# Optimization experiments

Measured on AMD Instinct MI355X. Metric: run time of the kernel, lower is better.

The kernel has to match this reference:

```python
import jax, jax.numpy as jnp
import numpy as np

NPOINT = 1024
RADIUS = 0.2
NSAMPLE = 32
MLP = (64, 64, 128)
EPS = 1e-5  # torch BatchNorm2d default


def farthest_point_sample(xyz, npoint):
    """xyz: [B,N,3] -> centroid indices [B,npoint] (deterministic start at index 0)."""
    B, N, _ = xyz.shape

    def step(carry, _):
        distance, farthest = carry  # [B,N], [B]
        centroid = jnp.take_along_axis(xyz, farthest[:, None, None], axis=1)  # [B,1,3]
        dist = jnp.sum((xyz - centroid) ** 2, axis=-1)  # [B,N]
        distance = jnp.minimum(distance, dist)
        new_farthest = jnp.argmax(distance, axis=-1)
        return (distance, new_farthest), farthest

    init = (jnp.full((B, N), 1e10, xyz.dtype), jnp.zeros((B,), jnp.int32))
    _, centroids = jax.lax.scan(step, init, None, length=npoint)  # [npoint,B]
    return centroids.T  # [B,npoint]


def ball_query(xyz, new_xyz, radius, nsample):
    """xyz:[B,N,3], new_xyz:[B,M,3] -> group_idx [B,M,nsample]."""
    N = xyz.shape[1]
    # sqrdists[b,m,n] = ||new_xyz[b,m] - xyz[b,n]||^2
    sqrdists = jnp.sum((new_xyz[:, :, None, :] - xyz[:, None, :, :]) ** 2, axis=-1)  # [B,M,N]
    idx = jnp.where(sqrdists > radius * radius, N, jnp.arange(N, dtype=jnp.int32))
    idx = jnp.sort(idx, axis=-1)[:, :, :nsample]
    return jnp.where(idx == N, 0, idx)  # out-of-ball slots fall back to point 0 (as in source)


def index_points(points, idx):
    """points:[B,N,C], idx:[B,M,K] -> [B,M,K,C]."""
    B, M, K = idx.shape
    flat = idx.reshape(B, M * K)
    out = jnp.take_along_axis(points, flat[:, :, None], axis=1)
    return out.reshape(B, M, K, points.shape[-1])


def _forward(xyz, points, layers):
    B = xyz.shape[0]
    fps_idx = farthest_point_sample(xyz, NPOINT)
    new_xyz = jnp.take_along_axis(xyz, fps_idx[:, :, None], axis=1)  # [B,M,3]
    group_idx = ball_query(xyz, new_xyz, RADIUS, NSAMPLE)  # [B,M,K]
    grouped_xyz = index_points(xyz, group_idx) - new_xyz[:, :, None, :]  # [B,M,K,3]
    x = jnp.concatenate([grouped_xyz, index_points(points, group_idx)], axis=-1)  # [B,M,K,3+C]
    # shared MLP: 1x1 conv + BatchNorm (training-mode batch stats) + ReLU
    for (w, b, g, be) in layers:
        x = jnp.einsum('bmkc,oc->bmko', x, w) + b
        mean = jnp.mean(x, axis=(0, 1, 2))
        var = jnp.var(x, axis=(0, 1, 2))  # biased, matches torch BN normalization
        x = jax.nn.relu(g * (x - mean) * jax.lax.rsqrt(var + EPS) + be)
    new_points = jnp.max(x, axis=2)  # [B,M,Cout]
    return new_xyz, new_points


def setup_inputs() -> dict:
    key = jax.random.key(0)
    ks = jax.random.split(key, 2 + len(MLP))
    B, N, C = 16, 4096, 64
    inp = {
        'xyz': jax.random.uniform(ks[0], (B, N, 3), jnp.float32),
        'points': jax.random.normal(ks[1], (B, N, C), jnp.float32),
    }
    last = 3 + C
    for i, out_ch in enumerate(MLP):
        inp[f'w{i}'] = jax.random.normal(ks[2 + i], (out_ch, last), jnp.float32) / np.sqrt(last).astype(np.float32)
        inp[f'b{i}'] = jnp.zeros((out_ch,), jnp.float32)
        inp[f'g{i}'] = jnp.ones((out_ch,), jnp.float32)
        inp[f'be{i}'] = jnp.zeros((out_ch,), jnp.float32)
        last = out_ch
    return inp


def reference(xyz, points, w0, b0, g0, be0, w1, b1, g1, be1, w2, b2, g2, be2):
    layers = [(w0, b0, g0, be0), (w1, b1, g1, be1), (w2, b2, g2, be2)]
    return _forward(xyz, points, layers)
```

## Files before the change

kernel.cpp:

```cpp
#include <hip/hip_runtime.h>

typedef unsigned int uint;
typedef unsigned short ushort;
typedef unsigned long long u64;

#define N_PTS 4096
#define B_SZ 16
#define M_PTS 1024
#define K_SMP 32
#define NROWS (B_SZ*M_PTS*K_SMP)
#define INV_CNT (1.0f/524288.0f)

__device__ __forceinline__ float sqdist3(float ax,float ay,float az,float bx,float by,float bz){
  float dx=__fsub_rn(ax,bx), dy=__fsub_rn(ay,by), dz=__fsub_rn(az,bz);
  return __fadd_rn(__fadd_rn(__fmul_rn(dx,dx),__fmul_rn(dy,dy)),__fmul_rn(dz,dz));
}
__device__ __forceinline__ ushort f2bf(float x){
  uint u = __float_as_uint(x);
  u = (u + 0x7fffu + ((u>>16)&1u)) >> 16;
  return (ushort)u;
}
__device__ __forceinline__ float bf2f(uint u){ return __uint_as_float(u<<16); }

__device__ __forceinline__ void kmerge(uint& kl, uint& kh, uint okl, uint okh){
  u64 a = ((u64)kh << 32) | kl;
  u64 b = ((u64)okh << 32) | okl;
  bool t = b > a;
  kl = t ? okl : kl;
  kh = t ? okh : kh;
}
template<int CTRL>
__device__ __forceinline__ uint dppu(uint v){
  return (uint)__builtin_amdgcn_update_dpp((int)v, (int)v, CTRL, 0xf, 0xf, false);
}
template<int CTRL>
__device__ __forceinline__ void dppkmerge(uint& kl, uint& kh){
  uint okl = dppu<CTRL>(kl);
  uint okh = dppu<CTRL>(kh);
  kmerge(kl, kh, okl, okh);
}

__global__ __launch_bounds__(512, 2) void fps_kernel(const float* __restrict__ xyz,
                                                     float* __restrict__ out_newxyz){
  const int b = blockIdx.x;
  const int t = threadIdx.x;
  __shared__ float4 sxyz[N_PTS];
  __shared__ uint   xch[2][8][2];
  const float* src = xyz + (size_t)b*N_PTS*3;
  float px[8], py[8], pz[8], dist[8];
  uint nl[8];
#pragma unroll
  for (int i=0;i<8;i++){
    const int p = t + 512*i;
    float x = src[3*p+0], y = src[3*p+1], z = src[3*p+2];
    px[i]=x; py[i]=y; pz[i]=z;
    dist[i]=1e10f; nl[i] = ~(uint)p;
    sxyz[p] = make_float4(x, y, z, 0.f);
  }
  __syncthreads();
  float cx, cy, cz;
  { float4 c0 = sxyz[0]; cx=c0.x; cy=c0.y; cz=c0.z; }
  const int w = t >> 6, lane = t & 63;
  float* outx = out_newxyz + (size_t)b*M_PTS*3;
  for (int s = 0; s < M_PTS; ++s){
    if (t == 0){ outx[s*3+0]=cx; outx[s*3+1]=cy; outx[s*3+2]=cz; }
    uint khv[8];
#pragma unroll
    for (int i=0;i<8;i++){
      float d  = sqdist3(px[i],py[i],pz[i],cx,cy,cz);
      float nd = fminf(dist[i], d);
      dist[i] = nd;
      khv[i] = __float_as_uint(nd);
    }
    uint l0=nl[0], h0=khv[0]; kmerge(l0,h0,nl[1],khv[1]);
    uint l1=nl[2], h1=khv[2]; kmerge(l1,h1,nl[3],khv[3]);
    uint l2=nl[4], h2=khv[4]; kmerge(l2,h2,nl[5],khv[5]);
    uint l3=nl[6], h3=khv[6]; kmerge(l3,h3,nl[7],khv[7]);
    kmerge(l0,h0,l1,h1); kmerge(l2,h2,l3,h3); kmerge(l0,h0,l2,h2);
    uint al=l0, ah=h0;
    dppkmerge<0x111>(al, ah);
    dppkmerge<0x112>(al, ah);
    dppkmerge<0x114>(al, ah);
    dppkmerge<0x118>(al, ah);
    dppkmerge<0x142>(al, ah);
    dppkmerge<0x143>(al, ah);
    const int par = s & 1;
    if (lane == 63){ xch[par][w][0] = al; xch[par][w][1] = ah; }
    __syncthreads();
    uint ckl = xch[par][lane & 7][0];
    uint ckh = xch[par][lane & 7][1];
    dppkmerge<0x111>(ckl, ckh);
    dppkmerge<0x112>(ckl, ckh);
    dppkmerge<0x114>(ckl, ckh);
    uint wkl = (uint)__builtin_amdgcn_readlane((int)ckl, 7);
    uint idx = ~wkl;
    float4 cc = sxyz[idx];
    cx = cc.x; cy = cc.y; cz = cc.z;
  }
}

__global__ __launch_bounds__(256) void ballq_kernel(const float* __restrict__ xyz,
                                                    const float* __restrict__ newxyz,
                                                    int* __restrict__ gidx){
  const int blk = blockIdx.x;
  const int b = blk >> 6;
  const int mbase = (blk & 63) * 16;
  __shared__ float sx[N_PTS], sy[N_PTS], sz[N_PTS];
  const float* src = xyz + (size_t)b*N_PTS*3;
  for (int i = threadIdx.x; i < N_PTS*3; i += 256){
    float v = src[i]; int p = i/3, j = i%3;
    (j==0?sx:(j==1?sy:sz))[p] = v;
  }
  __syncthreads();
  const int w = threadIdx.x >> 6, lane = threadIdx.x & 63;
  const float R2 = (float)(0.2*0.2);
  for (int mm = w; mm < 16; mm += 4){
    const int m = mbase + mm;
    const float* c = newxyz + ((size_t)b*M_PTS + m)*3;
    float cx = c[0], cy = c[1], cz = c[2];
    int* gout = gidx + ((size_t)b*M_PTS + m)*K_SMP;
    int cnt = 0;
    for (int base = 0; base < N_PTS && cnt < K_SMP; base += 64){
      int p = base + lane;
      float d = sqdist3(sx[p],sy[p],sz[p],cx,cy,cz);
      bool in = (d <= R2);
      unsigned long long mask = __ballot(in);
      int prefix = __popcll(mask & ((1ull << lane) - 1ull));
      int slot = cnt + prefix;
      if (in && slot < K_SMP) gout[slot] = p;
      cnt += __popcll(mask);
    }
    if (cnt < K_SMP){
      int slot = cnt + lane;
      if (slot < K_SMP) gout[slot] = 0;
    }
  }
}

__global__ __launch_bounds__(256, 2) void conv0_kernel(const float* __restrict__ xyz,
                                                       const float* __restrict__ points,
                                                       const float* __restrict__ newxyz,
                                                       const int* __restrict__ gidx,
                                                       const float* __restrict__ W0,
                                                       const float* __restrict__ b0,
                                                       ushort* __restrict__ x1){
  __shared__ float A [67][132];
  __shared__ float Bw[67][68];
  __shared__ float sb[64];
  const int tid = threadIdx.x;
  if (tid < 64) sb[tid] = b0[tid];
  for (int idx = tid; idx < 64*67; idx += 256){
    int o = idx / 67, k = idx - o*67;
    Bw[k][o] = W0[idx];
  }
  const size_t rbase = (size_t)blockIdx.x * 128;
  {
    const int r  = tid & 127;
    const int hf = tid >> 7;
    const int R = (int)rbase + r;
    const int b_ = R >> 15, m_ = (R >> 5) & 1023;
    const int g_ = gidx[R];
    const float4* p4 = (const float4*)(points + (((size_t)(b_<<12) + g_) << 6) + hf*32);
#pragma unroll
    for (int j=0;j<8;j++){
      float4 v = p4[j];
      int c = 3 + hf*32 + j*4;
      A[c+0][r]=v.x; A[c+1][r]=v.y; A[c+2][r]=v.z; A[c+3][r]=v.w;
    }
    if (hf == 0){
      const float* pc = newxyz + ((size_t)(b_<<10) + m_)*3;
      const float* pp = xyz    + ((size_t)(b_<<12) + g_)*3;
      A[0][r] = pp[0]-pc[0];
      A[1][r] = pp[1]-pc[1];
      A[2][r] = pp[2]-pc[2];
    }
  }
  __syncthreads();
  const int tr = tid >> 4, tc = tid & 15;
  float acc[8][4];
#pragma unroll
  for (int i=0;i<8;i++)
#pragma unroll
    for (int j=0;j<4;j++) acc[i][j] = sb[tc*4+j];
#pragma unroll 4
  for (int k=0;k<67;k++){
    float4 a0 = *(const float4*)&A [k][tr*8];
    float4 a1 = *(const float4*)&A [k][tr*8+4];
    float4 w  = *(const float4*)&Bw[k][tc*4];
    float av[8] = {a0.x,a0.y,a0.z,a0.w,a1.x,a1.y,a1.z,a1.w};
#pragma unroll
    for (int i=0;i<8;i++){
      acc[i][0]=fmaf(av[i],w.x,acc[i][0]);
      acc[i][1]=fmaf(av[i],w.y,acc[i][1]);
      acc[i][2]=fmaf(av[i],w.z,acc[i][2]);
      acc[i][3]=fmaf(av[i],w.w,acc[i][3]);
    }
  }
#pragma unroll
  for (int i=0;i<8;i++){
    uint2 v;
    v.x = (uint)f2bf(acc[i][0]) | ((uint)f2bf(acc[i][1])<<16);
    v.y = (uint)f2bf(acc[i][2]) | ((uint)f2bf(acc[i][3])<<16);
    *(uint2*)(x1 + ((rbase + tr*8 + i) << 6) + tc*4) = v;
  }
}

__global__ __launch_bounds__(256, 2) void convg64_kernel(const ushort* __restrict__ xin,
                                                         const float* __restrict__ Sv,
                                                         const float* __restrict__ SSv,
                                                         const float* __restrict__ gg,
                                                         const float* __restrict__ be,
                                                         const float* __restrict__ W,
                                                         const float* __restrict__ bias,
                                                         ushort* __restrict__ xout){
  __shared__ float A [64][132];
  __shared__ float Bw[64][68];
  __shared__ float sc[64], sh[64], sb[64];
  const int tid = threadIdx.x;
  if (tid < 64){
    int c = tid;
    float mean = Sv[c]*INV_CNT;
    float var  = fmaf(-mean, mean, SSv[c]*INV_CNT);
    float is   = rsqrtf(var + 1e-5f);
    float scv  = gg[c]*is;
    sc[c] = scv; sh[c] = fmaf(-mean, scv, be[c]);
    sb[c] = bias[c];
  }
  {
    const int o  = tid & 63;
    const int kq = tid >> 6;
    const float* wrow = W + (size_t)o*64 + kq*16;
#pragma unroll
    for (int q=0;q<4;q++){
      float4 wv = *(const float4*)(wrow + q*4);
      int k = kq*16 + q*4;
      Bw[k+0][o]=wv.x; Bw[k+1][o]=wv.y; Bw[k+2][o]=wv.z; Bw[k+3][o]=wv.w;
    }
  }
  __syncthreads();
  const size_t rbase = (size_t)blockIdx.x * 128;
  {
    const int r  = tid & 127;
    const int kh = tid >> 7;
    const uint4* src = (const uint4*)(xin + ((rbase + r) << 6) + kh*32);
#pragma unroll
    for (int g=0; g<4; g++){
      uint4 v = src[g];
      uint d[4] = {v.x,v.y,v.z,v.w};
#pragma unroll
      for (int q=0;q<4;q++){
        int k = kh*32 + g*8 + 2*q;
        float a0 = bf2f(d[q] & 0xffffu), a1 = bf2f(d[q] >> 16);
        A[k+0][r] = fmaxf(fmaf(a0, sc[k+0], sh[k+0]), 0.f);
        A[k+1][r] = fmaxf(fmaf(a1, sc[k+1], sh[k+1]), 0.f);
      }
    }
  }
  __syncthreads();
  const int tr = tid >> 4, tc = tid & 15;
  float acc[8][4];
#pragma unroll
  for (int i=0;i<8;i++)
#pragma unroll
    for (int j=0;j<4;j++) acc[i][j] = sb[tc*4+j];
#pragma unroll 4
  for (int k=0;k<64;k++){
    float4 a0 = *(const float4*)&A [k][tr*8];
    float4 a1 = *(const float4*)&A [k][tr*8+4];
    float4 w  = *(const float4*)&Bw[k][tc*4];
    float av[8] = {a0.x,a0.y,a0.z,a0.w,a1.x,a1.y,a1.z,a1.w};
#pragma unroll
    for (int i=0;i<8;i++){
      acc[i][0]=fmaf(av[i],w.x,acc[i][0]);
      acc[i][1]=fmaf(av[i],w.y,acc[i][1]);
      acc[i][2]=fmaf(av[i],w.z,acc[i][2]);
      acc[i][3]=fmaf(av[i],w.w,acc[i][3]);
    }
  }
#pragma unroll
  for (int i=0;i<8;i++){
    uint2 v;
    v.x = (uint)f2bf(acc[i][0]) | ((uint)f2bf(acc[i][1])<<16);
    v.y = (uint)f2bf(acc[i][2]) | ((uint)f2bf(acc[i][3])<<16);
    *(uint2*)(xout + ((rbase + tr*8 + i) << 6) + tc*4) = v;
  }
}

__global__ __launch_bounds__(256, 2) void convg128_kernel(const ushort* __restrict__ xin,
                                                          const float* __restrict__ Sv,
                                                          const float* __restrict__ SSv,
                                                          const float* __restrict__ gg,
                                                          const float* __restrict__ be,
                                                          const float* __restrict__ W,
                                                          const float* __restrict__ bias,
                                                          ushort* __restrict__ xout){
  __shared__ float A [64][132];
  __shared__ float Bw[64][132];
  __shared__ float sc[64], sh[64], sb[128];
  const int tid = threadIdx.x;
  if (tid < 64){
    int c = tid;
    float mean = Sv[c]*INV_CNT;
    float var  = fmaf(-mean, mean, SSv[c]*INV_CNT);
    float is   = rsqrtf(var + 1e-5f);
    float scv  = gg[c]*is;
    sc[c] = scv; sh[c] = fmaf(-mean, scv, be[c]);
  }
  if (tid < 128) sb[tid] = bias[tid];
  {
    const int o  = tid & 127;
    const int kh = tid >> 7;
    const float* wrow = W + (size_t)o*64 + kh*32;
#pragma unroll
    for (int q=0;q<8;q++){
      float4 wv = *(const float4*)(wrow + q*4);
      int k = kh*32 + q*4;
      Bw[k+0][o]=wv.x; Bw[k+1][o]=wv.y; Bw[k+2][o]=wv.z; Bw[k+3][o]=wv.w;
    }
  }
  __syncthreads();
  const size_t rbase = (size_t)blockIdx.x * 128;
  {
    const int r  = tid & 127;
    const int kh = tid >> 7;
    const uint4* src = (const uint4*)(xin + ((rbase + r) << 6) + kh*32);
#pragma unroll
    for (int g=0; g<4; g++){
      uint4 v = src[g];
      uint d[4] = {v.x,v.y,v.z,v.w};
#pragma unroll
      for (int q=0;q<4;q++){
        int k = kh*32 + g*8 + 2*q;
        float a0 = bf2f(d[q] & 0xffffu), a1 = bf2f(d[q] >> 16);
        A[k+0][r] = fmaxf(fmaf(a0, sc[k+0], sh[k+0]), 0.f);
        A[k+1][r] = fmaxf(fmaf(a1, sc[k+1], sh[k+1]), 0.f);
      }
    }
  }
  __syncthreads();
  const int tr = tid >> 4, tc = tid & 15;
  float acc[8][8];
#pragma unroll
  for (int i=0;i<8;i++)
#pragma unroll
    for (int j=0;j<8;j++) acc[i][j] = sb[tc*8+j];
#pragma unroll 2
  for (int k=0;k<64;k++){
    float4 a0 = *(const float4*)&A [k][tr*8];
    float4 a1 = *(const float4*)&A [k][tr*8+4];
    float4 w0 = *(const float4*)&Bw[k][tc*8];
    float4 w1 = *(const float4*)&Bw[k][tc*8+4];
    float av[8] = {a0.x,a0.y,a0.z,a0.w,a1.x,a1.y,a1.z,a1.w};
    float wv[8] = {w0.x,w0.y,w0.z,w0.w,w1.x,w1.y,w1.z,w1.w};
#pragma unroll
    for (int i=0;i<8;i++)
#pragma unroll
      for (int j=0;j<8;j++)
        acc[i][j] = fmaf(av[i], wv[j], acc[i][j]);
  }
#pragma unroll
  for (int i=0;i<8;i++){
    uint4 v;
    v.x = (uint)f2bf(acc[i][0]) | ((uint)f2bf(acc[i][1])<<16);
    v.y = (uint)f2bf(acc[i][2]) | ((uint)f2bf(acc[i][3])<<16);
    v.z = (uint)f2bf(acc[i][4]) | ((uint)f2bf(acc[i][5])<<16);
    v.w = (uint)f2bf(acc[i][6]) | ((uint)f2bf(acc[i][7])<<16);
    *(uint4*)(xout + ((rbase + tr*8 + i) << 7) + tc*8) = v;
  }
}

template<int C>
__global__ __launch_bounds__(256) void stats_kernel(const ushort* __restrict__ x,
                                                    float* __restrict__ S,
                                                    float* __restrict__ SS){
  constexpr int GRP = C/8;
  constexpr int RL  = 256/GRP;
  const int cg = threadIdx.x % GRP;
  const int rl = threadIdx.x / GRP;
  const int rows_per_block = NROWS / 1024;
  const int r0 = blockIdx.x * rows_per_block;
  float s[8], ss[8];
#pragma unroll
  for (int j=0;j<8;j++){ s[j]=0.f; ss[j]=0.f; }
  for (int r = r0 + rl; r < r0 + rows_per_block; r += RL){
    uint4 v = *(const uint4*)(x + (size_t)r*C + cg*8);
    uint d[4] = {v.x, v.y, v.z, v.w};
#pragma unroll
    for (int q=0;q<4;q++){
      float a0 = bf2f(d[q] & 0xffffu), a1 = bf2f(d[q] >> 16);
      s[2*q]   += a0; ss[2*q]   = fmaf(a0, a0, ss[2*q]);
      s[2*q+1] += a1; ss[2*q+1] = fmaf(a1, a1, ss[2*q+1]);
    }
  }
  __shared__ float ls[256][8], lss[256][8];
#pragma unroll
  for (int j=0;j<8;j++){ ls[threadIdx.x][j]=s[j]; lss[threadIdx.x][j]=ss[j]; }
  __syncthreads();
  if (threadIdx.x < C){
    const int grp = threadIdx.x >> 3, j = threadIdx.x & 7;
    float a = 0.f, q2 = 0.f;
#pragma unroll
    for (int q = 0; q < RL; q++){ a += ls[q*GRP + grp][j]; q2 += lss[q*GRP + grp][j]; }
    atomicAdd(&S[threadIdx.x], a); atomicAdd(&SS[threadIdx.x], q2);
  }
}

__global__ __launch_bounds__(256) void maxpool_kernel(const ushort* __restrict__ x3,
                                                      const float* __restrict__ S2,
                                                      const float* __restrict__ SS2,
                                                      const float* __restrict__ g2,
                                                      const float* __restrict__ be2,
                                                      float* __restrict__ outp){
  const int lane = threadIdx.x & 63, wv = threadIdx.x >> 6;
  const int bm = blockIdx.x*4 + wv;
  const int c0 = lane*2, c1 = c0+1;
  float mean0 = S2[c0]*INV_CNT;
  float var0  = fmaf(-mean0, mean0, SS2[c0]*INV_CNT);
  float s0 = g2[c0]*rsqrtf(var0+1e-5f);
  float h0 = fmaf(-mean0, s0, be2[c0]);
  float mean1 = S2[c1]*INV_CNT;
  float var1  = fmaf(-mean1, mean1, SS2[c1]*INV_CNT);
  float s1 = g2[c1]*rsqrtf(var1+1e-5f);
  float h1 = fmaf(-mean1, s1, be2[c1]);
  const uint* rb = (const uint*)(x3 + (size_t)bm*K_SMP*128);
  float mx0 = 0.f, mx1 = 0.f;
#pragma unroll
  for (int k=0;k<K_SMP;k++){
    uint v = rb[k*64 + lane];
    float a0 = bf2f(v & 0xffffu), a1 = bf2f(v >> 16);
    mx0 = fmaxf(mx0, fmaxf(fmaf(a0, s0, h0), 0.f));
    mx1 = fmaxf(mx1, fmaxf(fmaf(a1, s1, h1), 0.f));
  }
  float2* o2 = (float2*)(outp + (size_t)bm*128);
  o2[lane] = make_float2(mx0, mx1);
}

extern "C" void kernel_launch(void* const* d_in, const int* in_sizes, int n_in,
                              void* d_out, int out_size, void* d_ws, size_t ws_size,
                              hipStream_t stream){
  const float* xyz    = (const float*)d_in[0];
  const float* points = (const float*)d_in[1];
  const float* w0  = (const float*)d_in[2];
  const float* b0  = (const float*)d_in[3];
  const float* g0  = (const float*)d_in[4];
  const float* be0 = (const float*)d_in[5];
  const float* w1  = (const float*)d_in[6];
  const float* b1  = (const float*)d_in[7];
  const float* g1  = (const float*)d_in[8];
  const float* be1 = (const float*)d_in[9];
  const float* w2  = (const float*)d_in[10];
  const float* b2  = (const float*)d_in[11];
  const float* g2  = (const float*)d_in[12];
  const float* be2 = (const float*)d_in[13];

  float* out      = (float*)d_out;
  float* newxyz   = out;
  float* outp     = out + (size_t)B_SZ*M_PTS*3;

  char* ws = (char*)d_ws;
  int*   gidx  = (int*)ws;
  float* stats = (float*)(ws + (2u<<20));
  float* S0 = stats,      *SS0 = stats+64;
  float* S1 = stats+128,  *SS1 = stats+192;
  float* S2 = stats+256,  *SS2 = stats+384;
  ushort* x1 = (ushort*)(ws + (4u<<20));
  ushort* x3 = (ushort*)(ws + (4u<<20));
  ushort* x2 = (ushort*)(ws + (4u<<20) + 134217728u);

  hipMemsetAsync(stats, 0, 512*sizeof(float), stream);
  fps_kernel  <<<B_SZ, 512, 0, stream>>>(xyz, newxyz);
  ballq_kernel<<<1024, 256, 0, stream>>>(xyz, newxyz, gidx);
  conv0_kernel<<<NROWS/128, 256, 0, stream>>>(xyz, points, newxyz, gidx, w0, b0, x1);
  stats_kernel<64><<<1024, 256, 0, stream>>>(x1, S0, SS0);
  convg64_kernel<<<NROWS/128, 256, 0, stream>>>(x1, S0, SS0, g0, be0, w1, b1, x2);
  stats_kernel<64><<<1024, 256, 0, stream>>>(x2, S1, SS1);
  convg128_kernel<<<NROWS/128, 256, 0, stream>>>(x2, S1, SS1, g1, be1, w2, b2, x3);
  stats_kernel<128><<<1024, 256, 0, stream>>>(x3, S2, SS2);
  maxpool_kernel<<<NROWS/128, 256, 0, stream>>>(x3, S2, SS2, g2, be2, outp);
}
```

Measured before the change: 1.102 ms.

## Fuse BN stats into conv kernels and simplify FPS argmax reduction

The BatchNorm sum and sum-of-squares for the first two layers are now accumulated in the conv0 and convg64 epilogues from the bf16-rounded outputs and reduced with shuffles, shared memory and atomics. This removes two separate stats kernels that each re-read a large intermediate tensor. FPS also changes: each thread now owns 8 contiguous points loaded with float4 reads, and the per-step argmax uses a float max reduction plus a ballot and readlane instead of 64-bit packed key merges. Ties are resolved by a first-index search, but float atomics make the stats summation order nondeterministic.

```diff
diff --git a/kernel.cpp b/kernel.cpp
--- a/kernel.cpp
+++ b/kernel.cpp
@@ -22,22 +22,22 @@
 }
 __device__ __forceinline__ float bf2f(uint u){ return __uint_as_float(u<<16); }
 
-__device__ __forceinline__ void kmerge(uint& kl, uint& kh, uint okl, uint okh){
-  u64 a = ((u64)kh << 32) | kl;
-  u64 b = ((u64)okh << 32) | okl;
-  bool t = b > a;
-  kl = t ? okl : kl;
-  kh = t ? okh : kh;
-}
 template<int CTRL>
 __device__ __forceinline__ uint dppu(uint v){
   return (uint)__builtin_amdgcn_update_dpp((int)v, (int)v, CTRL, 0xf, 0xf, false);
 }
 template<int CTRL>
-__device__ __forceinline__ void dppkmerge(uint& kl, uint& kh){
-  uint okl = dppu<CTRL>(kl);
-  uint okh = dppu<CTRL>(kh);
-  kmerge(kl, kh, okl, okh);
+__device__ __forceinline__ float dppmaxf(float v){
+  float o = __uint_as_float(dppu<CTRL>(__float_as_uint(v)));
+  return fmaxf(v, o);
+}
+template<int CTRL>
+__device__ __forceinline__ void dppscan(float& v, uint& i){
+  float ov = __uint_as_float(dppu<CTRL>(__float_as_uint(v)));
+  uint  oi = dppu<CTRL>(i);
+  bool tk = (ov >= v);
+  v = tk ? ov : v;
+  i = tk ? oi : i;
 }
 
 __global__ __launch_bounds__(512, 2) void fps_kernel(const float* __restrict__ xyz,
@@ -45,17 +45,23 @@
   const int b = blockIdx.x;
   const int t = threadIdx.x;
   __shared__ float4 sxyz[N_PTS];
-  __shared__ uint   xch[2][8][2];
+  __shared__ __align__(8) uint2 xch[2][8];
   const float* src = xyz + (size_t)b*N_PTS*3;
+  for (int i = t; i < N_PTS; i += 512)
+    sxyz[i] = make_float4(src[3*i], src[3*i+1], src[3*i+2], 0.f);
+  const int p0 = t*8;
   float px[8], py[8], pz[8], dist[8];
-  uint nl[8];
-#pragma unroll
-  for (int i=0;i<8;i++){
-    const int p = t + 512*i;
-    float x = src[3*p+0], y = src[3*p+1], z = src[3*p+2];
-    px[i]=x; py[i]=y; pz[i]=z;
-    dist[i]=1e10f; nl[i] = ~(uint)p;
-    sxyz[p] = make_float4(x, y, z, 0.f);
+  {
+    const float4* s4 = (const float4*)(src + 3*p0);
+    float4 v[6];
+#pragma unroll
+    for (int q=0;q<6;q++) v[q] = s4[q];
+    const float* f = (const float*)v;
+#pragma unroll
+    for (int i=0;i<8;i++){
+      px[i]=f[3*i]; py[i]=f[3*i+1]; pz[i]=f[3*i+2];
+      dist[i]=1e10f;
+    }
   }
   __syncthreads();
   float cx, cy, cz;
@@ -64,37 +70,43 @@
   float* outx = out_newxyz + (size_t)b*M_PTS*3;
   for (int s = 0; s < M_PTS; ++s){
     if (t == 0){ outx[s*3+0]=cx; outx[s*3+1]=cy; outx[s*3+2]=cz; }
-    uint khv[8];
 #pragma unroll
     for (int i=0;i<8;i++){
-      float d  = sqdist3(px[i],py[i],pz[i],cx,cy,cz);
-      float nd = fminf(dist[i], d);
-      dist[i] = nd;
-      khv[i] = __float_as_uint(nd);
-    }
-    uint l0=nl[0], h0=khv[0]; kmerge(l0,h0,nl[1],khv[1]);
-    uint l1=nl[2], h1=khv[2]; kmerge(l1,h1,nl[3],khv[3]);
-    uint l2=nl[4], h2=khv[4]; kmerge(l2,h2,nl[5],khv[5]);
-    uint l3=nl[6], h3=khv[6]; kmerge(l3,h3,nl[7],khv[7]);
-    kmerge(l0,h0,l1,h1); kmerge(l2,h2,l3,h3); kmerge(l0,h0,l2,h2);
-    uint al=l0, ah=h0;
-    dppkmerge<0x111>(al, ah);
-    dppkmerge<0x112>(al, ah);
-    dppkmerge<0x114>(al, ah);
-    dppkmerge<0x118>(al, ah);
-    dppkmerge<0x142>(al, ah);
-    dppkmerge<0x143>(al, ah);
+      float d = sqdist3(px[i],py[i],pz[i],cx,cy,cz);
+      dist[i] = fminf(dist[i], d);
+    }
+    float m8 = fmaxf(fmaxf(fmaxf(dist[0],dist[1]), fmaxf(dist[2],dist[3])),
+                     fmaxf(fmaxf(dist[4],dist[5]), fmaxf(dist[6],dist[7])));
+    uint li = 7;
+    if (dist[6] == m8) li = 6;
+    if (dist[5] == m8) li = 5;
+    if (dist[4] == m8) li = 4;
+    if (dist[3] == m8) li = 3;
+    if (dist[2] == m8) li = 2;
+    if (dist[1] == m8) li = 1;
+    if (dist[0] == m8) li = 0;
+    const uint gi = (uint)p0 + li;
+    float wm = m8;
+    wm = dppmaxf<0x111>(wm);
+    wm = dppmaxf<0x112>(wm);
+    wm = dppmaxf<0x114>(wm);
+    wm = dppmaxf<0x118>(wm);
+    wm = dppmaxf<0x142>(wm);
+    wm = dppmaxf<0x143>(wm);
+    const float M = __uint_as_float((uint)__builtin_amdgcn_readlane((int)__float_as_uint(wm), 63));
+    unsigned long long blt = __ballot(m8 == M);
+    const int ll = __builtin_ctzll(blt);
+    const uint widx = (uint)__builtin_amdgcn_readlane((int)gi, ll);
     const int par = s & 1;
-    if (lane == 63){ xch[par][w][0] = al; xch[par][w][1] = ah; }
+    if (lane == 63) xch[par][w] = make_uint2(__float_as_uint(M), widx);
     __syncthreads();
-    uint ckl = xch[par][lane & 7][0];
-    uint ckh = xch[par][lane & 7][1];
-    dppkmerge<0x111>(ckl, ckh);
-    dppkmerge<0x112>(ckl, ckh);
-    dppkmerge<0x114>(ckl, ckh);
-    uint wkl = (uint)__builtin_amdgcn_readlane((int)ckl, 7);
-    uint idx = ~wkl;
-    float4 cc = sxyz[idx];
+    uint2 cw = xch[par][lane & 7];
+    float cv = __uint_as_float(cw.x); uint ci = cw.y;
+    dppscan<0x111>(cv, ci);
+    dppscan<0x112>(cv, ci);
+    dppscan<0x114>(cv, ci);
+    uint fi = (uint)__builtin_amdgcn_readlane((int)ci, 7);
+    float4 cc = sxyz[fi];
     cx = cc.x; cy = cc.y; cz = cc.z;
   }
 }
@@ -137,16 +149,40 @@
   }
 }
 
+__device__ __forceinline__ void conv_stats64(float s[4], float q[4], float (*sred)[16][8],
+                                             int tid, float* S, float* SS){
+  const int lane = tid & 63, w = tid >> 6, tc = tid & 15;
+#pragma unroll
+  for (int j=0;j<4;j++){
+    s[j] += __shfl_xor(s[j], 16); s[j] += __shfl_xor(s[j], 32);
+    q[j] += __shfl_xor(q[j], 16); q[j] += __shfl_xor(q[j], 32);
+  }
+  if (lane < 16){
+#pragma unroll
+    for (int j=0;j<4;j++){ sred[w][tc][j] = s[j]; sred[w][tc][4+j] = q[j]; }
+  }
+  __syncthreads();
+  if (tid < 64){
+    const int tcg = tid >> 2, j = tid & 3;
+    float a = sred[0][tcg][j]   + sred[1][tcg][j]   + sred[2][tcg][j]   + sred[3][tcg][j];
+    float b = sred[0][tcg][4+j] + sred[1][tcg][4+j] + sred[2][tcg][4+j] + sred[3][tcg][4+j];
+    atomicAdd(&S[tid], a); atomicAdd(&SS[tid], b);
+  }
+}
+
 __global__ __launch_bounds__(256, 2) void conv0_kernel(const float* __restrict__ xyz,
                                                        const float* __restrict__ points,
                                                        const float* __restrict__ newxyz,
                                                        const int* __restrict__ gidx,
                                                        const float* __restrict__ W0,
                                                        const float* __restrict__ b0,
-                                                       ushort* __restrict__ x1){
+                                                       ushort* __restrict__ x1,
+                                                       float* __restrict__ S0,
+                                                       float* __restrict__ SS0){
   __shared__ float A [67][132];
   __shared__ float Bw[67][68];
   __shared__ float sb[64];
+  __shared__ float sred[4][16][8];
   const int tid = threadIdx.x;
   if (tid < 64) sb[tid] = b0[tid];
   for (int idx = tid; idx < 64*67; idx += 256){
@@ -196,13 +232,21 @@
       acc[i][3]=fmaf(av[i],w.w,acc[i][3]);
     }
   }
+  float s[4] = {0.f,0.f,0.f,0.f}, q[4] = {0.f,0.f,0.f,0.f};
 #pragma unroll
   for (int i=0;i<8;i++){
     uint2 v;
     v.x = (uint)f2bf(acc[i][0]) | ((uint)f2bf(acc[i][1])<<16);
     v.y = (uint)f2bf(acc[i][2]) | ((uint)f2bf(acc[i][3])<<16);
     *(uint2*)(x1 + ((rbase + tr*8 + i) << 6) + tc*4) = v;
-  }
+    float v0=bf2f(v.x&0xffffu), v1=bf2f(v.x>>16), v2=bf2f(v.y&0xffffu), v3=bf2f(v.y>>16);
+    s[0]+=v0; q[0]=fmaf(v0,v0,q[0]);
+    s[1]+=v1; q[1]=fmaf(v1,v1,q[1]);
+    s[2]+=v2; q[2]=fmaf(v2,v2,q[2]);
+    s[3]+=v3; q[3]=fmaf(v3,v3,q[3]);
+  }
+  __syncthreads();
+  conv_stats64(s, q, sred, tid, S0, SS0);
 }
 
 __global__ __launch_bounds__(256, 2) void convg64_kernel(const ushort* __restrict__ xin,
@@ -212,10 +256,13 @@
                                                          const float* __restrict__ be,
                                                          const float* __restrict__ W,
                                                          const float* __restrict__ bias,
-                                                         ushort* __restrict__ xout){
+                                                         ushort* __restrict__ xout,
+                                                         float* __restrict__ S1,
+                                                         float* __restrict__ SS1){
   __shared__ float A [64][132];
   __shared__ float Bw[64][68];
   __shared__ float sc[64], sh[64], sb[64];
+  __shared__ float sred[4][16][8];
   const int tid = threadIdx.x;
   if (tid < 64){
     int c = tid;
@@ -277,13 +324,21 @@
       acc[i][3]=fmaf(av[i],w.w,acc[i][3]);
     }
   }
+  float s[4] = {0.f,0.f,0.f,0.f}, q[4] = {0.f,0.f,0.f,0.f};
 #pragma unroll
   for (int i=0;i<8;i++){
     uint2 v;
     v.x = (uint)f2bf(acc[i][0]) | ((uint)f2bf(acc[i][1])<<16);
     v.y = (uint)f2bf(acc[i][2]) | ((uint)f2bf(acc[i][3])<<16);
     *(uint2*)(xout + ((rbase + tr*8 + i) << 6) + tc*4) = v;
-  }
+    float v0=bf2f(v.x&0xffffu), v1=bf2f(v.x>>16), v2=bf2f(v.y&0xffffu), v3=bf2f(v.y>>16);
+    s[0]+=v0; q[0]=fmaf(v0,v0,q[0]);
+    s[1]+=v1; q[1]=fmaf(v1,v1,q[1]);
+    s[2]+=v2; q[2]=fmaf(v2,v2,q[2]);
+    s[3]+=v3; q[3]=fmaf(v3,v3,q[3]);
+  }
+  __syncthreads();
+  conv_stats64(s, q, sred, tid, S1, SS1);
 }
 
 __global__ __launch_bounds__(256, 2) void convg128_kernel(const ushort* __restrict__ xin,
@@ -470,10 +525,8 @@
   hipMemsetAsync(stats, 0, 512*sizeof(float), stream);
   fps_kernel  <<<B_SZ, 512, 0, stream>>>(xyz, newxyz);
   ballq_kernel<<<1024, 256, 0, stream>>>(xyz, newxyz, gidx);
-  conv0_kernel<<<NROWS/128, 256, 0, stream>>>(xyz, points, newxyz, gidx, w0, b0, x1);
-  stats_kernel<64><<<1024, 256, 0, stream>>>(x1, S0, SS0);
-  convg64_kernel<<<NROWS/128, 256, 0, stream>>>(x1, S0, SS0, g0, be0, w1, b1, x2);
-  stats_kernel<64><<<1024, 256, 0, stream>>>(x2, S1, SS1);
+  conv0_kernel<<<NROWS/128, 256, 0, stream>>>(xyz, points, newxyz, gidx, w0, b0, x1, S0, SS0);
+  convg64_kernel<<<NROWS/128, 256, 0, stream>>>(x1, S0, SS0, g0, be0, w1, b1, x2, S1, SS1);
   convg128_kernel<<<NROWS/128, 256, 0, stream>>>(x2, S1, SS1, g1, be1, w2, b2, x3);
   stats_kernel<128><<<1024, 256, 0, stream>>>(x3, S2, SS2);
   maxpool_kernel<<<NROWS/128, 256, 0, stream>>>(x3, S2, SS2, g2, be2, outp);
```

After: 1.112 ms. No clear change (+0.8%).
